# Kernel tuning notes

Hardware: AMD Instinct MI355X
Metric: run time of the kernel (lower is better)

## Reference

```python
import jax, jax.numpy as jnp
import numpy as np

SEGMENT_LENGTHS = [2048, 4096, 8192]
DILATION_RATES = [1, 2, 4]
EPS = 1e-8


def setup_inputs() -> dict:
    key = jax.random.key(0)
    kq, kk, kv = jax.random.split(key, 3)
    shape = (4, 8192, 8, 64)  # (b, n, h, d)
    return {
        "query": jax.random.normal(kq, shape, dtype=jnp.float32),
        "key": jax.random.normal(kk, shape, dtype=jnp.float32),
        "value": jax.random.normal(kv, shape, dtype=jnp.float32),
    }


def _dilated_attention(query, key, value):
    b, n, h, d = query.shape
    ng = len(SEGMENT_LENGTHS)
    group_sizes = [h // ng] * ng
    for i in range(h % ng):
        group_sizes[i] += 1
    scale = 1.0 / (d ** 0.5)  # torch SDPA default: 1/sqrt(E), E = last dim

    out = jnp.zeros_like(query)
    for i, (g, r, s) in enumerate(zip(group_sizes, DILATION_RATES, SEGMENT_LENGTHS)):
        offset = i % r
        hmin = sum(group_sizes[:i])
        hmax = hmin + g
        nseg = n // s
        # (b, nseg, s, h, d) -> strided dilation slice + head-group slice
        qg = query.reshape(b, nseg, s, h, d)[:, :, offset::r, hmin:hmax, :]
        kg = key.reshape(b, nseg, s, h, d)[:, :, offset::r, hmin:hmax, :]
        vg = value.reshape(b, nseg, s, h, d)[:, :, offset::r, hmin:hmax, :]
        # Faithful to the torch code: SDPA is fed (bn, s, h, d) untransposed, so
        # attention is over the HEAD axis (length g); s is a batch-like axis.
        scores = jnp.einsum('bnsqd,bnskd->bnsqk', qg, kg) * scale  # (b,nseg,sd,g,g)
        attn = jax.nn.softmax(scores, axis=-1)
        x = jnp.einsum('bnsqk,bnskd->bnsqd', attn, vg)  # (b,nseg,sd,g,d)
        # custom sum-normalization over (segment, dilated-position) dims
        x = x / (x.sum(axis=(1, 2), keepdims=True) + EPS)
        # scatter-add back into the strided/head-sliced locations
        out = (out.reshape(b, nseg, s, h, d)
                  .at[:, :, offset::r, hmin:hmax, :].add(x)
                  .reshape(b, n, h, d))
    return out / ng


def reference(query, key, value):
    return _dilated_attention(query, key, value)
```

## Files before the change

kernel.cpp:

```cpp
#include <hip/hip_runtime.h>
#include <math.h>

#define NB 4
#define NN 8192
#define NH 8
#define ND 64
#define NPART_STRIDE 192
#define N_BLOCKS_P1 1792
#define N_WAVES_P1  (N_BLOCKS_P1 * 4)


template<int G, int IT>
__device__ __forceinline__ void pass1_work(
    const float* __restrict__ Q, const float* __restrict__ K,
    const float* __restrict__ V, float* __restrict__ out,
    float* __restrict__ partials,
    int b, int chunk, int r, int off, int hmin, int seglen)
{
    const int tid  = threadIdx.x;
    const int w    = tid >> 6;
    const int lane = tid & 63;
    const int sg   = lane >> 4;
    const int l    = lane & 15;

    size_t rowbase[IT];
    #pragma unroll
    for (int it = 0; it < IT; ++it) {
        const int j   = chunk * (16 * IT) + w * (4 * IT) + it * 4 + sg;
        const int seg = j >> 11;
        const int td  = j & 2047;
        const int pos = seg * seglen + off + td * r;
        rowbase[it] = (((size_t)b * NN + pos) * NH + hmin) * ND + 4 * l;
    }

    float4 qv[IT][G], kv[IT][G], vv[IT][G];
    #pragma unroll
    for (int it = 0; it < IT; ++it)
        #pragma unroll
        for (int q = 0; q < G; ++q) {
            qv[it][q] = *(const float4*)(Q + rowbase[it] + q * ND);
            kv[it][q] = *(const float4*)(K + rowbase[it] + q * ND);
            vv[it][q] = *(const float4*)(V + rowbase[it] + q * ND);
        }

    float xs[G][4];
    #pragma unroll
    for (int q = 0; q < G; ++q)
        #pragma unroll
        for (int e = 0; e < 4; ++e) xs[q][e] = 0.f;

    #pragma unroll
    for (int it = 0; it < IT; ++it) {
        float sc[G][G];
        #pragma unroll
        for (int q = 0; q < G; ++q)
            #pragma unroll
            for (int k = 0; k < G; ++k)
                sc[q][k] = qv[it][q].x * kv[it][k].x + qv[it][q].y * kv[it][k].y
                         + qv[it][q].z * kv[it][k].z + qv[it][q].w * kv[it][k].w;

        #pragma unroll
        for (int o = 8; o >= 1; o >>= 1)
            #pragma unroll
            for (int q = 0; q < G; ++q)
                #pragma unroll
                for (int k = 0; k < G; ++k)
                    sc[q][k] += __shfl_xor(sc[q][k], o);

        #pragma unroll
        for (int q = 0; q < G; ++q) {
            float m = -INFINITY;
            #pragma unroll
            for (int k = 0; k < G; ++k) { sc[q][k] *= 0.125f; m = fmaxf(m, sc[q][k]); }
            float a[G]; float ssum = 0.f;
            #pragma unroll
            for (int k = 0; k < G; ++k) { a[k] = __expf(sc[q][k] - m); ssum += a[k]; }
            const float rs = 1.f / ssum;
            float xe0 = 0.f, xe1 = 0.f, xe2 = 0.f, xe3 = 0.f;
            #pragma unroll
            for (int k = 0; k < G; ++k) {
                const float aw = a[k] * rs;
                xe0 += aw * vv[it][k].x; xe1 += aw * vv[it][k].y;
                xe2 += aw * vv[it][k].z; xe3 += aw * vv[it][k].w;
            }
            *(float4*)(out + rowbase[it] + (size_t)q * ND) =
                make_float4(xe0, xe1, xe2, xe3);
            xs[q][0] += xe0; xs[q][1] += xe1; xs[q][2] += xe2; xs[q][3] += xe3;
        }
    }

    #pragma unroll
    for (int q = 0; q < G; ++q)
        #pragma unroll
        for (int e = 0; e < 4; ++e) {
            xs[q][e] += __shfl_xor(xs[q][e], 16);
            xs[q][e] += __shfl_xor(xs[q][e], 32);
        }

    if (lane < 16) {
        const int wid = blockIdx.x * 4 + w;
        #pragma unroll
        for (int q = 0; q < G; ++q)
            *(float4*)(partials + (size_t)wid * NPART_STRIDE + q * 64 + 4 * l) =
                make_float4(xs[q][0], xs[q][1], xs[q][2], xs[q][3]);
    }
}

__global__ __launch_bounds__(256)
void sda_pass1(const float* __restrict__ Q, const float* __restrict__ K,
               const float* __restrict__ V, float* __restrict__ out,
               float* __restrict__ partials)
{
    const int bid = blockIdx.x;
    if (bid < 1024) {
        const int b = bid >> 8, chunk = bid & 255;
        pass1_work<3, 2>(Q, K, V, out, partials, b, chunk, 1, 0, 0, 2048);
    } else if (bid < 1536) {
        const int loc = bid - 1024;
        const int b = loc >> 7, chunk = loc & 127;
        pass1_work<3, 2>(Q, K, V, out, partials, b, chunk, 2, 1, 3, 4096);
    } else {
        const int loc = bid - 1536;
        const int b = loc >> 6, chunk = loc & 63;
        pass1_work<2, 2>(Q, K, V, out, partials, b, chunk, 4, 2, 6, 8192);
    }
}

__global__ __launch_bounds__(256)
void sda_pass2a(const float* __restrict__ partials, float* __restrict__ partial2)
{
    const int bid   = blockIdx.x;
    const int bh    = bid >> 3;
    const int slice = bid & 7;
    const int b     = bh >> 3;
    const int h     = bh & 7;
    const int d     = threadIdx.x & 63;
    const int part  = threadIdx.x >> 6;
    int qi, wstart, cnt;
    if (h < 3)      { qi = h;     wstart = b * 1024;       cnt = 1024; }
    else if (h < 6) { qi = h - 3; wstart = 4096 + b * 512; cnt = 512;  }
    else            { qi = h - 6; wstart = 6144 + b * 256; cnt = 256;  }
    const int len = cnt >> 3;
    const int c0  = wstart + slice * len;
    float s = 0.f;
    #pragma unroll 4
    for (int c = part; c < len; c += 4)
        s += partials[(size_t)(c0 + c) * NPART_STRIDE + qi * 64 + d];
    __shared__ float sred[4][64];
    sred[part][d] = s;
    __syncthreads();
    if (part == 0)
        partial2[(size_t)bid * 64 + d] = sred[0][d] + sred[1][d] + sred[2][d] + sred[3][d];
}

__global__ __launch_bounds__(256)
void sda_pass2b(const float* __restrict__ partial2, float* __restrict__ inv)
{
    const int t = blockIdx.x * 256 + threadIdx.x;
    if (t >= NB * NH * ND) return;
    const int bh = t >> 6;
    const int d  = t & 63;
    float s = 0.f;
    #pragma unroll
    for (int sl = 0; sl < 8; ++sl)
        s += partial2[(size_t)(bh * 8 + sl) * 64 + d];
    inv[t] = 1.f / (3.f * (s + 1e-8f));
}

__global__ __launch_bounds__(256)
void sda_pass3(float* __restrict__ out, const float* __restrict__ inv)
{
    const int total4 = NB * NN * NH * ND / 4;
    for (int idx = blockIdx.x * 256 + threadIdx.x; idx < total4;
         idx += gridDim.x * 256) {
        const int d4  = idx & 15;
        const int rem = idx >> 4;
        const int h   = rem & 7;
        const int pos = (rem >> 3) & 8191;
        const int b   = rem >> 16;
        const bool cov = (h < 3) || ((h < 6) ? ((pos & 1) == 1) : ((pos & 3) == 2));
        float4 o;
        if (cov) {
            const float4 v = ((const float4*)out)[idx];
            const float4 f = ((const float4*)inv)[b * 128 + h * 16 + d4];
            o = make_float4(v.x * f.x, v.y * f.y, v.z * f.z, v.w * f.w);
        } else {
            o = make_float4(0.f, 0.f, 0.f, 0.f);
        }
        ((float4*)out)[idx] = o;
    }
}

extern "C" void kernel_launch(void* const* d_in, const int* in_sizes, int n_in,
                              void* d_out, int out_size, void* d_ws, size_t ws_size,
                              hipStream_t stream)
{
    const float* Q = (const float*)d_in[0];
    const float* K = (const float*)d_in[1];
    const float* V = (const float*)d_in[2];
    float* out      = (float*)d_out;
    float* partials = (float*)d_ws;
    float* partial2 = partials + (size_t)N_WAVES_P1 * NPART_STRIDE;
    float* inv      = partial2 + 256 * 64;

    hipLaunchKernelGGL(sda_pass1,  dim3(N_BLOCKS_P1), dim3(256), 0, stream,
                       Q, K, V, out, partials);
    hipLaunchKernelGGL(sda_pass2a, dim3(256), dim3(256), 0, stream, partials, partial2);
    hipLaunchKernelGGL(sda_pass2b, dim3(8),   dim3(256), 0, stream, partial2, inv);
    hipLaunchKernelGGL(sda_pass3,  dim3(2048), dim3(256), 0, stream, out, inv);
}
```

Before: 54.28 us.

## Stage Q/K/V through LDS with async global_load_lds and block-level partial reduction

Pass 1 now loads Q, K and V rows with global_load_lds directly into shared memory. It waits only for Q and K before computing scores and softmax, so the V loads overlap that compute. Each block handles one row group per wave instead of two, and the grid is doubled. Per-wave partial sums are reduced in LDS to one partial per block, which halves the partials read by pass 2a. The cost is extra LDS use (about 36KB per block), which may limit occupancy, plus a block barrier.

```diff
diff --git a/kernel.cpp b/kernel.cpp
--- a/kernel.cpp
+++ b/kernel.cpp
@@ -6,15 +6,21 @@
 #define NH 8
 #define ND 64
 #define NPART_STRIDE 192
-#define N_BLOCKS_P1 1792
-#define N_WAVES_P1  (N_BLOCKS_P1 * 4)
-
-
-template<int G, int IT>
+#define N_BLOCKS_P1 3584
+
+
+__device__ __forceinline__ void gload_lds16(const float* g, float* l) {
+    __builtin_amdgcn_global_load_lds(
+        (__attribute__((address_space(1))) void*)const_cast<float*>(g),
+        (__attribute__((address_space(3))) void*)l, 16, 0, 0);
+}
+
+template<int G>
 __device__ __forceinline__ void pass1_work(
     const float* __restrict__ Q, const float* __restrict__ K,
     const float* __restrict__ V, float* __restrict__ out,
     float* __restrict__ partials,
+    float (*stage)[9][256], float (*red)[3][64],
     int b, int chunk, int r, int off, int hmin, int seglen)
 {
     const int tid  = threadIdx.x;
@@ -23,70 +29,76 @@
     const int sg   = lane >> 4;
     const int l    = lane & 15;
 
-    size_t rowbase[IT];
-    #pragma unroll
-    for (int it = 0; it < IT; ++it) {
-        const int j   = chunk * (16 * IT) + w * (4 * IT) + it * 4 + sg;
-        const int seg = j >> 11;
-        const int td  = j & 2047;
-        const int pos = seg * seglen + off + td * r;
-        rowbase[it] = (((size_t)b * NN + pos) * NH + hmin) * ND + 4 * l;
-    }
-
-    float4 qv[IT][G], kv[IT][G], vv[IT][G];
-    #pragma unroll
-    for (int it = 0; it < IT; ++it)
-        #pragma unroll
-        for (int q = 0; q < G; ++q) {
-            qv[it][q] = *(const float4*)(Q + rowbase[it] + q * ND);
-            kv[it][q] = *(const float4*)(K + rowbase[it] + q * ND);
-            vv[it][q] = *(const float4*)(V + rowbase[it] + q * ND);
-        }
-
-    float xs[G][4];
+    const int j   = chunk * 16 + w * 4 + sg;
+    const int pos = (j >> 11) * seglen + off + (j & 2047) * r;
+    const size_t rowbase = (((size_t)b * NN + pos) * NH + hmin) * ND + 4 * l;
+
+    #pragma unroll
+    for (int q = 0; q < G; ++q) gload_lds16(Q + rowbase + q * ND, &stage[w][q][0]);
+    #pragma unroll
+    for (int q = 0; q < G; ++q) gload_lds16(K + rowbase + q * ND, &stage[w][3 + q][0]);
+    #pragma unroll
+    for (int q = 0; q < G; ++q) gload_lds16(V + rowbase + q * ND, &stage[w][6 + q][0]);
+
+    asm volatile("s_waitcnt vmcnt(%0)" :: "n"(G) : "memory");
+    __builtin_amdgcn_sched_barrier(0);
+
+    float4 qv[G], kv[G];
+    #pragma unroll
+    for (int q = 0; q < G; ++q) {
+        qv[q] = *(const float4*)&stage[w][q][4 * lane];
+        kv[q] = *(const float4*)&stage[w][3 + q][4 * lane];
+    }
+
+    float sc[G][G];
     #pragma unroll
     for (int q = 0; q < G; ++q)
         #pragma unroll
-        for (int e = 0; e < 4; ++e) xs[q][e] = 0.f;
-
-    #pragma unroll
-    for (int it = 0; it < IT; ++it) {
-        float sc[G][G];
+        for (int k = 0; k < G; ++k)
+            sc[q][k] = qv[q].x * kv[k].x + qv[q].y * kv[k].y
+                     + qv[q].z * kv[k].z + qv[q].w * kv[k].w;
+
+    #pragma unroll
+    for (int o = 8; o >= 1; o >>= 1)
         #pragma unroll
         for (int q = 0; q < G; ++q)
             #pragma unroll
             for (int k = 0; k < G; ++k)
-                sc[q][k] = qv[it][q].x * kv[it][k].x + qv[it][q].y * kv[it][k].y
-                         + qv[it][q].z * kv[it][k].z + qv[it][q].w * kv[it][k].w;
-
-        #pragma unroll
-        for (int o = 8; o >= 1; o >>= 1)
-            #pragma unroll
-            for (int q = 0; q < G; ++q)
-                #pragma unroll
-                for (int k = 0; k < G; ++k)
-                    sc[q][k] += __shfl_xor(sc[q][k], o);
-
-        #pragma unroll
-        for (int q = 0; q < G; ++q) {
-            float m = -INFINITY;
-            #pragma unroll
-            for (int k = 0; k < G; ++k) { sc[q][k] *= 0.125f; m = fmaxf(m, sc[q][k]); }
-            float a[G]; float ssum = 0.f;
-            #pragma unroll
-            for (int k = 0; k < G; ++k) { a[k] = __expf(sc[q][k] - m); ssum += a[k]; }
-            const float rs = 1.f / ssum;
-            float xe0 = 0.f, xe1 = 0.f, xe2 = 0.f, xe3 = 0.f;
-            #pragma unroll
-            for (int k = 0; k < G; ++k) {
-                const float aw = a[k] * rs;
-                xe0 += aw * vv[it][k].x; xe1 += aw * vv[it][k].y;
-                xe2 += aw * vv[it][k].z; xe3 += aw * vv[it][k].w;
-            }
-            *(float4*)(out + rowbase[it] + (size_t)q * ND) =
-                make_float4(xe0, xe1, xe2, xe3);
-            xs[q][0] += xe0; xs[q][1] += xe1; xs[q][2] += xe2; xs[q][3] += xe3;
+                sc[q][k] += __shfl_xor(sc[q][k], o);
+
+    #pragma unroll
+    for (int q = 0; q < G; ++q) {
+        float m = -INFINITY;
+        #pragma unroll
+        for (int k = 0; k < G; ++k) { sc[q][k] *= 0.125f; m = fmaxf(m, sc[q][k]); }
+        float ssum = 0.f;
+        #pragma unroll
+        for (int k = 0; k < G; ++k) { sc[q][k] = __expf(sc[q][k] - m); ssum += sc[q][k]; }
+        const float rs = 1.f / ssum;
+        #pragma unroll
+        for (int k = 0; k < G; ++k) sc[q][k] *= rs;
+    }
+
+    asm volatile("s_waitcnt vmcnt(0)" ::: "memory");
+    __builtin_amdgcn_sched_barrier(0);
+
+    float4 vv[G];
+    #pragma unroll
+    for (int q = 0; q < G; ++q)
+        vv[q] = *(const float4*)&stage[w][6 + q][4 * lane];
+
+    float xs[G][4];
+    #pragma unroll
+    for (int q = 0; q < G; ++q) {
+        float xe0 = 0.f, xe1 = 0.f, xe2 = 0.f, xe3 = 0.f;
+        #pragma unroll
+        for (int k = 0; k < G; ++k) {
+            const float aw = sc[q][k];
+            xe0 += aw * vv[k].x; xe1 += aw * vv[k].y;
+            xe2 += aw * vv[k].z; xe3 += aw * vv[k].w;
         }
+        *(float4*)(out + rowbase + (size_t)q * ND) = make_float4(xe0, xe1, xe2, xe3);
+        xs[q][0] = xe0; xs[q][1] = xe1; xs[q][2] = xe2; xs[q][3] = xe3;
     }
 
     #pragma unroll
@@ -97,12 +109,17 @@
             xs[q][e] += __shfl_xor(xs[q][e], 32);
         }
 
-    if (lane < 16) {
-        const int wid = blockIdx.x * 4 + w;
+    if (lane < 16)
         #pragma unroll
         for (int q = 0; q < G; ++q)
-            *(float4*)(partials + (size_t)wid * NPART_STRIDE + q * 64 + 4 * l) =
-                make_float4(xs[q][0], xs[q][1], xs[q][2], xs[q][3]);
+            *(float4*)&red[w][q][4 * l] = make_float4(xs[q][0], xs[q][1], xs[q][2], xs[q][3]);
+    __syncthreads();
+
+    if (tid < G * 64) {
+        const int q = tid >> 6;
+        const int d = tid & 63;
+        partials[(size_t)blockIdx.x * NPART_STRIDE + q * 64 + d] =
+            red[0][q][d] + red[1][q][d] + red[2][q][d] + red[3][q][d];
     }
 }
 
@@ -111,18 +128,20 @@
                const float* __restrict__ V, float* __restrict__ out,
                float* __restrict__ partials)
 {
+    __shared__ float stage[4][9][256];
+    __shared__ float red[4][3][64];
     const int bid = blockIdx.x;
-    if (bid < 1024) {
-        const int b = bid >> 8, chunk = bid & 255;
-        pass1_work<3, 2>(Q, K, V, out, partials, b, chunk, 1, 0, 0, 2048);
-    } else if (bid < 1536) {
-        const int loc = bid - 1024;
+    if (bid < 2048) {
+        const int b = bid >> 9, chunk = bid & 511;
+        pass1_work<3>(Q, K, V, out, partials, stage, red, b, chunk, 1, 0, 0, 2048);
+    } else if (bid < 3072) {
+        const int loc = bid - 2048;
+        const int b = loc >> 8, chunk = loc & 255;
+        pass1_work<3>(Q, K, V, out, partials, stage, red, b, chunk, 2, 1, 3, 4096);
+    } else {
+        const int loc = bid - 3072;
         const int b = loc >> 7, chunk = loc & 127;
-        pass1_work<3, 2>(Q, K, V, out, partials, b, chunk, 2, 1, 3, 4096);
-    } else {
-        const int loc = bid - 1536;
-        const int b = loc >> 6, chunk = loc & 63;
-        pass1_work<2, 2>(Q, K, V, out, partials, b, chunk, 4, 2, 6, 8192);
+        pass1_work<2>(Q, K, V, out, partials, stage, red, b, chunk, 4, 2, 6, 8192);
     }
 }
 
@@ -136,12 +155,12 @@
     const int h     = bh & 7;
     const int d     = threadIdx.x & 63;
     const int part  = threadIdx.x >> 6;
-    int qi, wstart, cnt;
-    if (h < 3)      { qi = h;     wstart = b * 1024;       cnt = 1024; }
-    else if (h < 6) { qi = h - 3; wstart = 4096 + b * 512; cnt = 512;  }
-    else            { qi = h - 6; wstart = 6144 + b * 256; cnt = 256;  }
+    int qi, bstart, cnt;
+    if (h < 3)      { qi = h;     bstart = b * 512;        cnt = 512; }
+    else if (h < 6) { qi = h - 3; bstart = 2048 + b * 256; cnt = 256; }
+    else            { qi = h - 6; bstart = 3072 + b * 128; cnt = 128; }
     const int len = cnt >> 3;
-    const int c0  = wstart + slice * len;
+    const int c0  = bstart + slice * len;
     float s = 0.f;
     #pragma unroll 4
     for (int c = part; c < len; c += 4)
@@ -200,7 +219,7 @@
     const float* V = (const float*)d_in[2];
     float* out      = (float*)d_out;
     float* partials = (float*)d_ws;
-    float* partial2 = partials + (size_t)N_WAVES_P1 * NPART_STRIDE;
+    float* partial2 = partials + (size_t)N_BLOCKS_P1 * NPART_STRIDE;
     float* inv      = partial2 + 256 * 64;
 
     hipLaunchKernelGGL(sda_pass1,  dim3(N_BLOCKS_P1), dim3(256), 0, stream,
```

New measurement: 53.26 us. No clear change (-1.9%).

## Remap pass1 lanes so each wave processes one position with lanes per query head

Applied to the files above, without the earlier changes.

Pass1 is reorganized so that each wave processes a single dilated position per iteration. Each 16-lane subgroup handles one query head (three heads, or two positions with two heads for the last group), instead of four positions with every lane computing all G×G scores. This cuts per-thread register arrays and shuffle counts (only G shuffles per reduction level) and removes the cross-subgroup partial-sum shuffle. The trade-off is that K and V are re-read by each query subgroup, the fourth subgroup is idle in the 3-head groups, and loads become serialized over an 8-step loop instead of being issued all up front.

```diff
diff --git a/kernel.cpp b/kernel.cpp
--- a/kernel.cpp
+++ b/kernel.cpp
@@ -5,105 +5,124 @@
 #define NN 8192
 #define NH 8
 #define ND 64
+#define ROWF (NH * ND)
 #define NPART_STRIDE 192
 #define N_BLOCKS_P1 1792
 #define N_WAVES_P1  (N_BLOCKS_P1 * 4)
 
 
-template<int G, int IT>
-__device__ __forceinline__ void pass1_work(
+__device__ __forceinline__ float dot4(float4 a, float4 b) {
+    return a.x * b.x + a.y * b.y + a.z * b.z + a.w * b.w;
+}
+
+template<int HOFF>
+__device__ __forceinline__ void pass1_g3(
     const float* __restrict__ Q, const float* __restrict__ K,
     const float* __restrict__ V, float* __restrict__ out,
     float* __restrict__ partials,
-    int b, int chunk, int r, int off, int hmin, int seglen)
-{
-    const int tid  = threadIdx.x;
-    const int w    = tid >> 6;
-    const int lane = tid & 63;
+    int b, int cw, int wid, int r, int off, int seglen)
+{
+    const int lane = threadIdx.x & 63;
     const int sg   = lane >> 4;
-    const int l    = lane & 15;
-
-    size_t rowbase[IT];
-    #pragma unroll
-    for (int it = 0; it < IT; ++it) {
-        const int j   = chunk * (16 * IT) + w * (4 * IT) + it * 4 + sg;
-        const int seg = j >> 11;
-        const int td  = j & 2047;
-        const int pos = seg * seglen + off + td * r;
-        rowbase[it] = (((size_t)b * NN + pos) * NH + hmin) * ND + 4 * l;
-    }
-
-    float4 qv[IT][G], kv[IT][G], vv[IT][G];
-    #pragma unroll
-    for (int it = 0; it < IT; ++it)
+    const int l15  = lane & 15;
+
+    float xs0 = 0.f, xs1 = 0.f, xs2 = 0.f, xs3 = 0.f;
+
+    #pragma unroll 2
+    for (int t = 0; t < 8; ++t) {
+        const int j   = cw * 8 + t;
+        const int pos = (j >> 11) * seglen + off + (j & 2047) * r;
+        const size_t rb = ((size_t)b * NN + pos) * ROWF;
+
+        const float4 qv = *(const float4*)(Q + rb + HOFF + 4 * lane);
+        const float4 k0 = *(const float4*)(K + rb + HOFF + 0 * ND + 4 * l15);
+        const float4 k1 = *(const float4*)(K + rb + HOFF + 1 * ND + 4 * l15);
+        const float4 k2 = *(const float4*)(K + rb + HOFF + 2 * ND + 4 * l15);
+        const float4 v0 = *(const float4*)(V + rb + HOFF + 0 * ND + 4 * l15);
+        const float4 v1 = *(const float4*)(V + rb + HOFF + 1 * ND + 4 * l15);
+        const float4 v2 = *(const float4*)(V + rb + HOFF + 2 * ND + 4 * l15);
+
+        float s0 = dot4(qv, k0), s1 = dot4(qv, k1), s2 = dot4(qv, k2);
         #pragma unroll
-        for (int q = 0; q < G; ++q) {
-            qv[it][q] = *(const float4*)(Q + rowbase[it] + q * ND);
-            kv[it][q] = *(const float4*)(K + rowbase[it] + q * ND);
-            vv[it][q] = *(const float4*)(V + rowbase[it] + q * ND);
+        for (int o = 8; o >= 1; o >>= 1) {
+            s0 += __shfl_xor(s0, o);
+            s1 += __shfl_xor(s1, o);
+            s2 += __shfl_xor(s2, o);
         }
 
-    float xs[G][4];
-    #pragma unroll
-    for (int q = 0; q < G; ++q)
+        s0 *= 0.125f; s1 *= 0.125f; s2 *= 0.125f;
+        const float m  = fmaxf(s0, fmaxf(s1, s2));
+        const float e0 = __expf(s0 - m), e1 = __expf(s1 - m), e2 = __expf(s2 - m);
+        const float rs = 1.f / (e0 + e1 + e2);
+        const float w0 = e0 * rs, w1 = e1 * rs, w2 = e2 * rs;
+
+        const float xe0 = w0 * v0.x + w1 * v1.x + w2 * v2.x;
+        const float xe1 = w0 * v0.y + w1 * v1.y + w2 * v2.y;
+        const float xe2 = w0 * v0.z + w1 * v1.z + w2 * v2.z;
+        const float xe3 = w0 * v0.w + w1 * v1.w + w2 * v2.w;
+
+        if (sg < 3)
+            *(float4*)(out + rb + HOFF + 4 * lane) = make_float4(xe0, xe1, xe2, xe3);
+        xs0 += xe0; xs1 += xe1; xs2 += xe2; xs3 += xe3;
+    }
+
+    if (sg < 3)
+        *(float4*)(partials + (size_t)wid * NPART_STRIDE + sg * 64 + 4 * l15) =
+            make_float4(xs0, xs1, xs2, xs3);
+}
+
+__device__ __forceinline__ void pass1_g2(
+    const float* __restrict__ Q, const float* __restrict__ K,
+    const float* __restrict__ V, float* __restrict__ out,
+    float* __restrict__ partials, int b, int cw, int wid)
+{
+    const int lane = threadIdx.x & 63;
+    const int half = lane >> 5;
+    const int sg2  = (lane >> 4) & 1;
+    const int l15  = lane & 15;
+    const int l31  = lane & 31;
+
+    float xs0 = 0.f, xs1 = 0.f, xs2 = 0.f, xs3 = 0.f;
+
+    #pragma unroll 2
+    for (int t = 0; t < 4; ++t) {
+        const int j   = cw * 8 + t * 2 + half;
+        const int pos = 2 + 4 * j;
+        const size_t rb = ((size_t)b * NN + pos) * ROWF + 384;
+
+        const float4 qv = *(const float4*)(Q + rb + 4 * l31);
+        const float4 k0 = *(const float4*)(K + rb + 0 * ND + 4 * l15);
+        const float4 k1 = *(const float4*)(K + rb + 1 * ND + 4 * l15);
+        const float4 v0 = *(const float4*)(V + rb + 0 * ND + 4 * l15);
+        const float4 v1 = *(const float4*)(V + rb + 1 * ND + 4 * l15);
+
+        float s0 = dot4(qv, k0), s1 = dot4(qv, k1);
         #pragma unroll
-        for (int e = 0; e < 4; ++e) xs[q][e] = 0.f;
-
-    #pragma unroll
-    for (int it = 0; it < IT; ++it) {
-        float sc[G][G];
-        #pragma unroll
-        for (int q = 0; q < G; ++q)
-            #pragma unroll
-            for (int k = 0; k < G; ++k)
-                sc[q][k] = qv[it][q].x * kv[it][k].x + qv[it][q].y * kv[it][k].y
-                         + qv[it][q].z * kv[it][k].z + qv[it][q].w * kv[it][k].w;
-
-        #pragma unroll
-        for (int o = 8; o >= 1; o >>= 1)
-            #pragma unroll
-            for (int q = 0; q < G; ++q)
-                #pragma unroll
-                for (int k = 0; k < G; ++k)
-                    sc[q][k] += __shfl_xor(sc[q][k], o);
-
-        #pragma unroll
-        for (int q = 0; q < G; ++q) {
-            float m = -INFINITY;
-            #pragma unroll
-            for (int k = 0; k < G; ++k) { sc[q][k] *= 0.125f; m = fmaxf(m, sc[q][k]); }
-            float a[G]; float ssum = 0.f;
-            #pragma unroll
-            for (int k = 0; k < G; ++k) { a[k] = __expf(sc[q][k] - m); ssum += a[k]; }
-            const float rs = 1.f / ssum;
-            float xe0 = 0.f, xe1 = 0.f, xe2 = 0.f, xe3 = 0.f;
-            #pragma unroll
-            for (int k = 0; k < G; ++k) {
-                const float aw = a[k] * rs;
-                xe0 += aw * vv[it][k].x; xe1 += aw * vv[it][k].y;
-                xe2 += aw * vv[it][k].z; xe3 += aw * vv[it][k].w;
-            }
-            *(float4*)(out + rowbase[it] + (size_t)q * ND) =
-                make_float4(xe0, xe1, xe2, xe3);
-            xs[q][0] += xe0; xs[q][1] += xe1; xs[q][2] += xe2; xs[q][3] += xe3;
+        for (int o = 8; o >= 1; o >>= 1) {
+            s0 += __shfl_xor(s0, o);
+            s1 += __shfl_xor(s1, o);
         }
-    }
-
-    #pragma unroll
-    for (int q = 0; q < G; ++q)
-        #pragma unroll
-        for (int e = 0; e < 4; ++e) {
-            xs[q][e] += __shfl_xor(xs[q][e], 16);
-            xs[q][e] += __shfl_xor(xs[q][e], 32);
-        }
-
-    if (lane < 16) {
-        const int wid = blockIdx.x * 4 + w;
-        #pragma unroll
-        for (int q = 0; q < G; ++q)
-            *(float4*)(partials + (size_t)wid * NPART_STRIDE + q * 64 + 4 * l) =
-                make_float4(xs[q][0], xs[q][1], xs[q][2], xs[q][3]);
-    }
+
+        s0 *= 0.125f; s1 *= 0.125f;
+        const float m  = fmaxf(s0, s1);
+        const float e0 = __expf(s0 - m), e1 = __expf(s1 - m);
+        const float rs = 1.f / (e0 + e1);
+        const float w0 = e0 * rs, w1 = e1 * rs;
+
+        const float xe0 = w0 * v0.x + w1 * v1.x;
+        const float xe1 = w0 * v0.y + w1 * v1.y;
+        const float xe2 = w0 * v0.z + w1 * v1.z;
+        const float xe3 = w0 * v0.w + w1 * v1.w;
+
+        *(float4*)(out + rb + 4 * l31) = make_float4(xe0, xe1, xe2, xe3);
+        xs0 += xe0; xs1 += xe1; xs2 += xe2; xs3 += xe3;
+    }
+
+    xs0 += __shfl_xor(xs0, 32); xs1 += __shfl_xor(xs1, 32);
+    xs2 += __shfl_xor(xs2, 32); xs3 += __shfl_xor(xs3, 32);
+    if (half == 0)
+        *(float4*)(partials + (size_t)wid * NPART_STRIDE + sg2 * 64 + 4 * l15) =
+            make_float4(xs0, xs1, xs2, xs3);
 }
 
 __global__ __launch_bounds__(256)
@@ -112,17 +131,19 @@
                float* __restrict__ partials)
 {
     const int bid = blockIdx.x;
+    const int w   = threadIdx.x >> 6;
+    const int wid = bid * 4 + w;
     if (bid < 1024) {
-        const int b = bid >> 8, chunk = bid & 255;
-        pass1_work<3, 2>(Q, K, V, out, partials, b, chunk, 1, 0, 0, 2048);
+        const int b = bid >> 8, cw = (bid & 255) * 4 + w;
+        pass1_g3<0>(Q, K, V, out, partials, b, cw, wid, 1, 0, 2048);
     } else if (bid < 1536) {
         const int loc = bid - 1024;
-        const int b = loc >> 7, chunk = loc & 127;
-        pass1_work<3, 2>(Q, K, V, out, partials, b, chunk, 2, 1, 3, 4096);
+        const int b = loc >> 7, cw = (loc & 127) * 4 + w;
+        pass1_g3<192>(Q, K, V, out, partials, b, cw, wid, 2, 1, 4096);
     } else {
         const int loc = bid - 1536;
-        const int b = loc >> 6, chunk = loc & 63;
-        pass1_work<2, 2>(Q, K, V, out, partials, b, chunk, 4, 2, 6, 8192);
+        const int b = loc >> 6, cw = (loc & 63) * 4 + w;
+        pass1_g2(Q, K, V, out, partials, b, cw, wid);
     }
 }
 
```

New measurement: 57.72 us. 1.06x slower.

## Process 32 rows per wave with 8 lanes per row and fewer blocks

Applied to the files above, without the earlier changes.

Pass 1 now maps 8 lanes to each row of 64 dims, with each lane loading two float4s, instead of 16 lanes with one float4. Each wave loops over 4 iterations of 8 rows, so the grid shrinks from 1792 to 448 blocks and the partial-sum count drops fourfold, which pass 2a indexes accordingly. V loads are deferred until after the softmax to lower register pressure, and the score reduction needs one fewer shuffle step. The smaller grid on a many-CU GPU may reduce memory-level parallelism and occupancy for this bandwidth-bound pass.

```diff
diff --git a/kernel.cpp b/kernel.cpp
--- a/kernel.cpp
+++ b/kernel.cpp
@@ -6,61 +6,55 @@
 #define NH 8
 #define ND 64
 #define NPART_STRIDE 192
-#define N_BLOCKS_P1 1792
-#define N_WAVES_P1  (N_BLOCKS_P1 * 4)
-
-
-template<int G, int IT>
+#define N_BLOCKS_P1 448
+#define N_WAVES_P1  1792
+
+
+__device__ __forceinline__ float dot4(float4 a, float4 b) {
+    return a.x * b.x + a.y * b.y + a.z * b.z + a.w * b.w;
+}
+
+template<int G>
 __device__ __forceinline__ void pass1_work(
     const float* __restrict__ Q, const float* __restrict__ K,
     const float* __restrict__ V, float* __restrict__ out,
     float* __restrict__ partials,
-    int b, int chunk, int r, int off, int hmin, int seglen)
-{
-    const int tid  = threadIdx.x;
-    const int w    = tid >> 6;
-    const int lane = tid & 63;
-    const int sg   = lane >> 4;
-    const int l    = lane & 15;
-
-    size_t rowbase[IT];
+    int b, int wave_local, int wid, int r, int off, int hmin, int seglen)
+{
+    const int lane = threadIdx.x & 63;
+    const int p8   = lane >> 3;
+    const int d8   = lane & 7;
+
+    float4 xs[G][2];
     #pragma unroll
-    for (int it = 0; it < IT; ++it) {
-        const int j   = chunk * (16 * IT) + w * (4 * IT) + it * 4 + sg;
-        const int seg = j >> 11;
-        const int td  = j & 2047;
-        const int pos = seg * seglen + off + td * r;
-        rowbase[it] = (((size_t)b * NN + pos) * NH + hmin) * ND + 4 * l;
-    }
-
-    float4 qv[IT][G], kv[IT][G], vv[IT][G];
-    #pragma unroll
-    for (int it = 0; it < IT; ++it)
-        #pragma unroll
-        for (int q = 0; q < G; ++q) {
-            qv[it][q] = *(const float4*)(Q + rowbase[it] + q * ND);
-            kv[it][q] = *(const float4*)(K + rowbase[it] + q * ND);
-            vv[it][q] = *(const float4*)(V + rowbase[it] + q * ND);
-        }
-
-    float xs[G][4];
-    #pragma unroll
-    for (int q = 0; q < G; ++q)
-        #pragma unroll
-        for (int e = 0; e < 4; ++e) xs[q][e] = 0.f;
-
-    #pragma unroll
-    for (int it = 0; it < IT; ++it) {
+    for (int q = 0; q < G; ++q) {
+        xs[q][0] = make_float4(0.f, 0.f, 0.f, 0.f);
+        xs[q][1] = make_float4(0.f, 0.f, 0.f, 0.f);
+    }
+
+    #pragma unroll 2
+    for (int t = 0; t < 4; ++t) {
+        const int j   = wave_local * 32 + t * 8 + p8;
+        const int pos = (j >> 11) * seglen + off + (j & 2047) * r;
+        const size_t rb = (((size_t)b * NN + pos) * NH + hmin) * ND + 8 * d8;
+
+        float4 qv[G][2], kv[G][2];
+        #pragma unroll
+        for (int q = 0; q < G; ++q) {
+            qv[q][0] = *(const float4*)(Q + rb + q * ND);
+            qv[q][1] = *(const float4*)(Q + rb + q * ND + 4);
+            kv[q][0] = *(const float4*)(K + rb + q * ND);
+            kv[q][1] = *(const float4*)(K + rb + q * ND + 4);
+        }
+
         float sc[G][G];
         #pragma unroll
         for (int q = 0; q < G; ++q)
             #pragma unroll
             for (int k = 0; k < G; ++k)
-                sc[q][k] = qv[it][q].x * kv[it][k].x + qv[it][q].y * kv[it][k].y
-                         + qv[it][q].z * kv[it][k].z + qv[it][q].w * kv[it][k].w;
-
-        #pragma unroll
-        for (int o = 8; o >= 1; o >>= 1)
+                sc[q][k] = dot4(qv[q][0], kv[k][0]) + dot4(qv[q][1], kv[k][1]);
+        #pragma unroll
+        for (int o = 4; o >= 1; o >>= 1)
             #pragma unroll
             for (int q = 0; q < G; ++q)
                 #pragma unroll
@@ -72,37 +66,56 @@
             float m = -INFINITY;
             #pragma unroll
             for (int k = 0; k < G; ++k) { sc[q][k] *= 0.125f; m = fmaxf(m, sc[q][k]); }
-            float a[G]; float ssum = 0.f;
-            #pragma unroll
-            for (int k = 0; k < G; ++k) { a[k] = __expf(sc[q][k] - m); ssum += a[k]; }
+            float ssum = 0.f;
+            #pragma unroll
+            for (int k = 0; k < G; ++k) { sc[q][k] = __expf(sc[q][k] - m); ssum += sc[q][k]; }
             const float rs = 1.f / ssum;
-            float xe0 = 0.f, xe1 = 0.f, xe2 = 0.f, xe3 = 0.f;
+            #pragma unroll
+            for (int k = 0; k < G; ++k) sc[q][k] *= rs;
+        }
+
+        float4 vv[G][2];
+        #pragma unroll
+        for (int q = 0; q < G; ++q) {
+            vv[q][0] = *(const float4*)(V + rb + q * ND);
+            vv[q][1] = *(const float4*)(V + rb + q * ND + 4);
+        }
+
+        #pragma unroll
+        for (int q = 0; q < G; ++q) {
+            float4 x0 = make_float4(0.f, 0.f, 0.f, 0.f);
+            float4 x1 = make_float4(0.f, 0.f, 0.f, 0.f);
             #pragma unroll
             for (int k = 0; k < G; ++k) {
-                const float aw = a[k] * rs;
-                xe0 += aw * vv[it][k].x; xe1 += aw * vv[it][k].y;
-                xe2 += aw * vv[it][k].z; xe3 += aw * vv[it][k].w;
+                const float aw = sc[q][k];
+                x0.x += aw * vv[k][0].x; x0.y += aw * vv[k][0].y;
+                x0.z += aw * vv[k][0].z; x0.w += aw * vv[k][0].w;
+                x1.x += aw * vv[k][1].x; x1.y += aw * vv[k][1].y;
+                x1.z += aw * vv[k][1].z; x1.w += aw * vv[k][1].w;
             }
-            *(float4*)(out + rowbase[it] + (size_t)q * ND) =
-                make_float4(xe0, xe1, xe2, xe3);
-            xs[q][0] += xe0; xs[q][1] += xe1; xs[q][2] += xe2; xs[q][3] += xe3;
+            *(float4*)(out + rb + q * ND)     = x0;
+            *(float4*)(out + rb + q * ND + 4) = x1;
+            xs[q][0].x += x0.x; xs[q][0].y += x0.y; xs[q][0].z += x0.z; xs[q][0].w += x0.w;
+            xs[q][1].x += x1.x; xs[q][1].y += x1.y; xs[q][1].z += x1.z; xs[q][1].w += x1.w;
         }
     }
 
     #pragma unroll
-    for (int q = 0; q < G; ++q)
-        #pragma unroll
-        for (int e = 0; e < 4; ++e) {
-            xs[q][e] += __shfl_xor(xs[q][e], 16);
-            xs[q][e] += __shfl_xor(xs[q][e], 32);
-        }
-
-    if (lane < 16) {
-        const int wid = blockIdx.x * 4 + w;
-        #pragma unroll
-        for (int q = 0; q < G; ++q)
-            *(float4*)(partials + (size_t)wid * NPART_STRIDE + q * 64 + 4 * l) =
-                make_float4(xs[q][0], xs[q][1], xs[q][2], xs[q][3]);
+    for (int o = 8; o <= 32; o <<= 1)
+        #pragma unroll
+        for (int q = 0; q < G; ++q) {
+            xs[q][0].x += __shfl_xor(xs[q][0].x, o); xs[q][0].y += __shfl_xor(xs[q][0].y, o);
+            xs[q][0].z += __shfl_xor(xs[q][0].z, o); xs[q][0].w += __shfl_xor(xs[q][0].w, o);
+            xs[q][1].x += __shfl_xor(xs[q][1].x, o); xs[q][1].y += __shfl_xor(xs[q][1].y, o);
+            xs[q][1].z += __shfl_xor(xs[q][1].z, o); xs[q][1].w += __shfl_xor(xs[q][1].w, o);
+        }
+
+    if (lane < 8) {
+        #pragma unroll
+        for (int q = 0; q < G; ++q) {
+            *(float4*)(partials + (size_t)wid * NPART_STRIDE + q * 64 + 8 * d8)     = xs[q][0];
+            *(float4*)(partials + (size_t)wid * NPART_STRIDE + q * 64 + 8 * d8 + 4) = xs[q][1];
+        }
     }
 }
 
@@ -112,17 +125,19 @@
                float* __restrict__ partials)
 {
     const int bid = blockIdx.x;
-    if (bid < 1024) {
-        const int b = bid >> 8, chunk = bid & 255;
-        pass1_work<3, 2>(Q, K, V, out, partials, b, chunk, 1, 0, 0, 2048);
-    } else if (bid < 1536) {
-        const int loc = bid - 1024;
-        const int b = loc >> 7, chunk = loc & 127;
-        pass1_work<3, 2>(Q, K, V, out, partials, b, chunk, 2, 1, 3, 4096);
+    const int w   = threadIdx.x >> 6;
+    const int wid = bid * 4 + w;
+    if (bid < 256) {
+        const int b = bid >> 6, wl = (bid & 63) * 4 + w;
+        pass1_work<3>(Q, K, V, out, partials, b, wl, wid, 1, 0, 0, 2048);
+    } else if (bid < 384) {
+        const int loc = bid - 256;
+        const int b = loc >> 5, wl = (loc & 31) * 4 + w;
+        pass1_work<3>(Q, K, V, out, partials, b, wl, wid, 2, 1, 3, 4096);
     } else {
-        const int loc = bid - 1536;
-        const int b = loc >> 6, chunk = loc & 63;
-        pass1_work<2, 2>(Q, K, V, out, partials, b, chunk, 4, 2, 6, 8192);
+        const int loc = bid - 384;
+        const int b = loc >> 4, wl = (loc & 15) * 4 + w;
+        pass1_work<2>(Q, K, V, out, partials, b, wl, wid, 4, 2, 6, 8192);
     }
 }
 
@@ -137,9 +152,9 @@
     const int d     = threadIdx.x & 63;
     const int part  = threadIdx.x >> 6;
     int qi, wstart, cnt;
-    if (h < 3)      { qi = h;     wstart = b * 1024;       cnt = 1024; }
-    else if (h < 6) { qi = h - 3; wstart = 4096 + b * 512; cnt = 512;  }
-    else            { qi = h - 6; wstart = 6144 + b * 256; cnt = 256;  }
+    if (h < 3)      { qi = h;     wstart = b * 256;        cnt = 256; }
+    else if (h < 6) { qi = h - 3; wstart = 1024 + b * 128; cnt = 128; }
+    else            { qi = h - 6; wstart = 1536 + b * 64;  cnt = 64;  }
     const int len = cnt >> 3;
     const int c0  = wstart + slice * len;
     float s = 0.f;
```

Result: no change. 53.32 us (-1.8%).
